# Kernel optimization log

Hardware: AMD Instinct MI355X
Metric: run time of the kernel (lower is better)

## Reference

```python
import jax, jax.numpy as jnp
import numpy as np

PRE_NMS_TOPK = 6000
POST_NMS_TOPK = 1000
NMS_THRESH = 0.7
MIN_SIZE = 16.0
N = 1_000_000
H, W = 800, 1333


def setup_inputs() -> dict:
    key = jax.random.key(0)
    ki, kx, ky, kw, kh, kd, kl = jax.random.split(key, 7)
    image = jax.random.normal(ki, (1, H, W, 3), jnp.float32)
    # realistic anchors: centers uniform over image, sizes in [8, 228)
    cx = jax.random.uniform(kx, (N,), jnp.float32) * W
    cy = jax.random.uniform(ky, (N,), jnp.float32) * H
    aw = jax.random.uniform(kw, (N,), jnp.float32) * 220.0 + 8.0
    ah = jax.random.uniform(kh, (N,), jnp.float32) * 220.0 + 8.0
    anchors = jnp.stack([cx - 0.5 * aw, cy - 0.5 * ah, cx + 0.5 * aw, cy + 0.5 * ah], axis=1)
    bbox_deltas = jax.random.normal(kd, (N, 4), jnp.float32) * 0.1
    logits = jax.random.normal(kl, (N, 1), jnp.float32)
    return {"image": image, "anchors": anchors, "bbox_deltas": bbox_deltas, "logits": logits}


def _iou_matrix(boxes):
    # boxes: [K,4] as (x1,y1,x2,y2); IoU is symmetric in axis labeling,
    # matching tf.image.non_max_suppression's overlap math.
    x1, y1, x2, y2 = boxes[:, 0], boxes[:, 1], boxes[:, 2], boxes[:, 3]
    area = (x2 - x1) * (y2 - y1)
    ix1 = jnp.maximum(x1[:, None], x1[None, :])
    iy1 = jnp.maximum(y1[:, None], y1[None, :])
    ix2 = jnp.minimum(x2[:, None], x2[None, :])
    iy2 = jnp.minimum(y2[:, None], y2[None, :])
    inter = jnp.maximum(ix2 - ix1, 0.0) * jnp.maximum(iy2 - iy1, 0.0)
    union = area[:, None] + area[None, :] - inter
    return jnp.where(union > 0.0, inter / union, 0.0)


def _sequential_nms(iou, valid, thresh):
    # iou: [K,K]; boxes are already sorted by descending score.
    K = iou.shape[0]
    idx = jnp.arange(K)

    def step(keep, inp):
        i, row = inp
        ki = keep[i]
        suppress = ki & (row > thresh) & (idx > i)
        return keep & ~suppress, ki

    _, kept = jax.lax.scan(step, valid, (idx, iou))
    return kept  # [K] bool, in sorted order


def reference(image, anchors, bbox_deltas, logits):
    height = jnp.float32(image.shape[1])
    width = jnp.float32(image.shape[2])

    # --- box decode ---
    wa = anchors[:, 2] - anchors[:, 0]
    ha = anchors[:, 3] - anchors[:, 1]
    xa = anchors[:, 0] + 0.5 * wa
    ya = anchors[:, 1] + 0.5 * ha
    x = bbox_deltas[:, 0] * wa + xa
    y = bbox_deltas[:, 1] * ha + ya
    w = jnp.exp(bbox_deltas[:, 2]) * wa
    h = jnp.exp(bbox_deltas[:, 3]) * ha
    x1 = jnp.clip(x - 0.5 * w, 0.0, width - 1.0)
    y1 = jnp.clip(y - 0.5 * h, 0.0, height - 1.0)
    x2 = jnp.clip(x + 0.5 * w, 0.0, width - 1.0)
    y2 = jnp.clip(y + 0.5 * h, 0.0, height - 1.0)
    proposals = jnp.stack([x1, y1, x2, y2], axis=1)  # [N,4]

    # --- min-size filter (mask instead of dynamic gather) ---
    valid = ((x2 - x1) >= MIN_SIZE) & ((y2 - y1) >= MIN_SIZE)
    scores = jnp.where(valid, jax.nn.sigmoid(logits[:, 0]), -jnp.inf)

    # --- pre-NMS top-k ---
    top_scores, top_idx = jax.lax.top_k(scores, PRE_NMS_TOPK)
    top_boxes = proposals[top_idx]              # [K,4]
    top_valid = top_scores > -jnp.inf

    # --- NMS ---
    iou = _iou_matrix(top_boxes)
    kept = _sequential_nms(iou, top_valid, NMS_THRESH)

    # --- pack kept boxes (in score order) into fixed [POST,4], zero-padded ---
    rank = jnp.cumsum(kept.astype(jnp.int32)) - 1
    slot = jnp.where(kept, rank, POST_NMS_TOPK)  # invalid -> dropped
    out = jnp.zeros((POST_NMS_TOPK, 4), top_boxes.dtype)
    out = out.at[slot].set(top_boxes, mode="drop")
    return out
```

## Files before the change

kernel.cpp:

```cpp
#include <hip/hip_runtime.h>
#include <stdint.h>
#include <math.h>

#define N_ANCH   1000000
#define N4       (N_ANCH / 4)
#define NBLK4    ((N4 + 1023) / 1024)
#define NBLK256  ((N4 + 255) / 256)
#define PRE_K    6000
#define POST_K   1000
#define WORDS    94
#define ROWS     6016
#define W_IMG    1333.0f
#define H_IMG    800.0f

#define NS       7168
#define RBLK     112

#define OFF_KEYS   0x000000u
#define OFF_HIST1  0x400000u
#define OFF_HIST2  0x404000u
#define OFF_CTRL   0x410000u
#define OFF_CAND   0x410100u
#define OFF_BOXES  0x41F000u
#define OFF_VALID  0x437000u
#define OFF_MASK   0x440000u

__device__ __forceinline__ float ref_exp(float v) {
  return (float)exp((double)v);
}

__device__ __forceinline__ void decode_box(float ax, float ay, float az, float aw,
                                           float dx, float dy, float dz, float dw,
                                           float& x1, float& y1, float& x2, float& y2,
                                           bool& valid) {
  float wa = __fsub_rn(az, ax);
  float ha = __fsub_rn(aw, ay);
  float xa = __fadd_rn(ax, __fmul_rn(0.5f, wa));
  float ya = __fadd_rn(ay, __fmul_rn(0.5f, ha));
  float x  = __fadd_rn(__fmul_rn(dx, wa), xa);
  float y  = __fadd_rn(__fmul_rn(dy, ha), ya);
  float w  = __fmul_rn(ref_exp(dz), wa);
  float h  = __fmul_rn(ref_exp(dw), ha);
  float hw = __fmul_rn(0.5f, w);
  float hh = __fmul_rn(0.5f, h);
  x1 = fminf(fmaxf(__fsub_rn(x, hw), 0.0f), W_IMG - 1.0f);
  y1 = fminf(fmaxf(__fsub_rn(y, hh), 0.0f), H_IMG - 1.0f);
  x2 = fminf(fmaxf(__fadd_rn(x, hw), 0.0f), W_IMG - 1.0f);
  y2 = fminf(fmaxf(__fadd_rn(y, hh), 0.0f), H_IMG - 1.0f);
  valid = (__fsub_rn(x2, x1) >= 16.0f) && (__fsub_rn(y2, y1) >= 16.0f);
}

__device__ __forceinline__ uint32_t wave_iscan(uint32_t x, int lane) {
  #pragma unroll
  for (int off = 1; off < 64; off <<= 1) {
    uint32_t u = __shfl_up(x, off, 64);
    if (lane >= off) x += u;
  }
  return x;
}

__device__ __forceinline__ uint64_t bcast64(uint64_t v, int lane) {
  uint32_t lo = (uint32_t)__builtin_amdgcn_readlane((int)(uint32_t)v, lane);
  uint32_t hi = (uint32_t)__builtin_amdgcn_readlane((int)(uint32_t)(v >> 32), lane);
  return ((uint64_t)hi << 32) | lo;
}

__global__ void __launch_bounds__(256) k_decode(const float4* __restrict__ anchors,
                                                const float4* __restrict__ deltas,
                                                const float*  __restrict__ logits,
                                                uint32_t* __restrict__ keys) {
  int i = blockIdx.x * 256 + threadIdx.x;
  if (i >= N_ANCH) return;
  float4 a = anchors[i];
  float4 d = deltas[i];
  float wa = a.z - a.x, ha = a.w - a.y;
  float xa = a.x + 0.5f * wa, ya = a.y + 0.5f * ha;
  float x = d.x * wa + xa, y = d.y * ha + ya;
  float w = __expf(d.z) * wa, h = __expf(d.w) * ha;
  float fx1 = fminf(fmaxf(x - 0.5f * w, 0.0f), W_IMG - 1.0f);
  float fx2 = fminf(fmaxf(x + 0.5f * w, 0.0f), W_IMG - 1.0f);
  float fy1 = fminf(fmaxf(y - 0.5f * h, 0.0f), H_IMG - 1.0f);
  float fy2 = fminf(fmaxf(y + 0.5f * h, 0.0f), H_IMG - 1.0f);
  float X = fx2 - fx1, Y = fy2 - fy1;
  bool valid = (X >= 16.0f) && (Y >= 16.0f);
  if (fabsf(X - 16.0f) < 0.02f || fabsf(Y - 16.0f) < 0.02f) {
    float ex1, ey1, ex2, ey2; bool vv;
    decode_box(a.x, a.y, a.z, a.w, d.x, d.y, d.z, d.w, ex1, ey1, ex2, ey2, vv);
    valid = vv;
  }
  uint32_t u = __float_as_uint(logits[i]);
  uint32_t o = (u & 0x80000000u) ? ~u : (u | 0x80000000u);
  keys[i] = valid ? ~o : 0xFFFFFFFFu;
}

__global__ void __launch_bounds__(1024) k_histA(const uint4* __restrict__ keys4,
                                                uint32_t* __restrict__ hist1) {
  __shared__ uint32_t lh[4096];
  int tid = threadIdx.x, lane = tid & 63;
  for (int b = tid; b < 4096; b += 1024) lh[b] = 0u;
  __syncthreads();
  int i4 = blockIdx.x * 1024 + tid;
  uint32_t invc = 0;
  if (i4 < N4) {
    uint4 kk = keys4[i4];
    uint32_t ks[4] = { kk.x, kk.y, kk.z, kk.w };
    #pragma unroll
    for (int e = 0; e < 4; e++) {
      if (ks[e] != 0xFFFFFFFFu) atomicAdd(&lh[ks[e] >> 20], 1u);
      else invc++;
    }
  }
  #pragma unroll
  for (int off = 32; off > 0; off >>= 1) invc += __shfl_down(invc, off, 64);
  if (lane == 0 && invc) atomicAdd(&lh[4095], invc);
  __syncthreads();
  for (int b = tid; b < 4096; b += 1024) {
    uint32_t cv = lh[b];
    if (cv) atomicAdd(&hist1[b], cv);
  }
}

__global__ void __launch_bounds__(1024) k_cut1(const uint32_t* __restrict__ hist1,
                                               uint32_t* __restrict__ ctrl) {
  __shared__ uint32_t part[1024];
  int t = threadIdx.x;
  uint4 s4 = ((const uint4*)hist1)[t];
  uint32_t tot = s4.x + s4.y + s4.z + s4.w;
  part[t] = tot;
  __syncthreads();
  uint32_t inc = tot;
  for (int off = 1; off < 1024; off <<= 1) {
    uint32_t u = (t >= off) ? part[t - off] : 0u;
    __syncthreads();
    inc += u;
    part[t] = inc;
    __syncthreads();
  }
  uint32_t ex = inc - tot;
  if (ex < PRE_K && inc >= PRE_K) {
    uint32_t run = ex;
    uint32_t binv[4] = { s4.x, s4.y, s4.z, s4.w };
    for (int b = 0; b < 4; b++) {
      if (run + binv[b] >= PRE_K) { ctrl[2] = 4 * t + b; ctrl[3] = run; break; }
      run += binv[b];
    }
  }
  if (t == 1023 && inc < PRE_K) { ctrl[2] = 4095u; ctrl[3] = inc; }
}

__global__ void __launch_bounds__(256) k_hist2(const uint4* __restrict__ keys4,
                                               const uint32_t* __restrict__ ctrl,
                                               uint32_t* __restrict__ hist2) {
  __shared__ uint32_t lh[256];
  int tid = threadIdx.x;
  lh[tid] = 0u;
  __syncthreads();
  uint32_t c = ctrl[2];
  int i4 = blockIdx.x * 256 + tid;
  if (i4 < N4) {
    uint4 kk = keys4[i4];
    uint32_t ks[4] = { kk.x, kk.y, kk.z, kk.w };
    #pragma unroll
    for (int e = 0; e < 4; e++)
      if ((ks[e] >> 20) == c) atomicAdd(&lh[(ks[e] >> 12) & 0xFFu], 1u);
  }
  __syncthreads();
  uint32_t v = lh[tid];
  if (v) atomicAdd(&hist2[tid], v);
}

__global__ void __launch_bounds__(64) k_cut2(const uint32_t* __restrict__ hist2,
                                             uint32_t* __restrict__ ctrl) {
  int lane = threadIdx.x;
  uint32_t c = ctrl[2], base = ctrl[3];
  const uint32_t* p = hist2 + 4 * lane;
  uint32_t b0 = p[0], b1 = p[1], b2 = p[2], b3 = p[3];
  uint32_t tot = b0 + b1 + b2 + b3;
  uint32_t inc = wave_iscan(tot, lane);
  uint32_t ex = inc - tot;
  bool found = false;
  if (base + ex < PRE_K && base + inc >= PRE_K) {
    uint32_t run = base + ex;
    uint32_t binv[4] = { b0, b1, b2, b3 };
    for (int b = 0; b < 4; b++) {
      if (run + binv[b] >= PRE_K) { ctrl[1] = (c << 8) | (uint32_t)(4 * lane + b); found = true; break; }
      run += binv[b];
    }
  }
  uint64_t fb = __ballot(found);
  if (lane == 0 && fb == 0ull) ctrl[1] = 0xFFFFFu;
}

__global__ void __launch_bounds__(256) k_compact(const uint4* __restrict__ keys4,
                                                 const float* __restrict__ logits,
                                                 uint32_t* ctrl,
                                                 uint64_t* __restrict__ cand) {
  __shared__ uint32_t wcnt[4];
  __shared__ uint32_t bbase_s;
  int tid = threadIdx.x, lane = tid & 63, wv = tid >> 6;
  uint32_t T = ctrl[1];
  int i4 = blockIdx.x * 256 + tid;
  uint4 kk = make_uint4(~0u, ~0u, ~0u, ~0u);
  if (i4 < N4) kk = keys4[i4];
  uint32_t ks[4] = { kk.x, kk.y, kk.z, kk.w };
  bool pass[4]; uint64_t m[4];
  uint32_t tot = 0;
  #pragma unroll
  for (int e = 0; e < 4; e++) {
    pass[e] = (i4 < N4) && ((ks[e] >> 12) <= T);
    m[e] = __ballot(pass[e]);
    tot += (uint32_t)__popcll((unsigned long long)m[e]);
  }
  if (lane == 0) wcnt[wv] = tot;
  __syncthreads();
  if (tid == 0) {
    uint32_t bt = wcnt[0] + wcnt[1] + wcnt[2] + wcnt[3];
    bbase_s = bt ? atomicAdd(&ctrl[0], bt) : 0u;
  }
  __syncthreads();
  uint32_t wb = bbase_s;
  for (int w2 = 0; w2 < wv; w2++) wb += wcnt[w2];
  uint64_t lmask = (1ull << lane) - 1ull;
  #pragma unroll
  for (int e = 0; e < 4; e++) {
    if (pass[e]) {
      int i = 4 * i4 + e;
      uint32_t skey;
      if (ks[e] == 0xFFFFFFFFu) {
        skey = 0xFF800000u;
      } else {
        double xd = (double)logits[i];
        float s = (float)(1.0 / (1.0 + exp(-xd)));
        skey = 0x7FFFFFFFu & ~__float_as_uint(s);
      }
      uint32_t p = wb + (uint32_t)__popcll((unsigned long long)(m[e] & lmask));
      if (p < NS) cand[p] = ((uint64_t)skey << 20) | (uint32_t)i;
    }
    wb += (uint32_t)__popcll((unsigned long long)m[e]);
  }
}

__global__ void __launch_bounds__(256) k_rank(
    const uint32_t* __restrict__ ctrl,
    const uint64_t* __restrict__ cand,
    const float4* __restrict__ anchors,
    const float4* __restrict__ deltas,
    float4* __restrict__ boxes,
    uint32_t* __restrict__ valid) {
  __shared__ uint32_t part[4][64];
  int tid = threadIdx.x;
  int wv = tid >> 6, lane = tid & 63;
  int i = blockIdx.x * 64 + lane;
  uint32_t M = ctrl[0]; if (M > NS) M = NS;
  uint64_t myk = (i < (int)M) ? cand[i] : ~0ull;
  uint32_t cnt = 0;
  const int QUART = NS / 4;
  int jbase = wv * QUART;
  for (int s = 0; s < QUART / 64; s++) {
    int j = jbase + s * 64 + lane;
    uint64_t c = (j < (int)M) ? cand[j] : ~0ull;
    #pragma unroll
    for (int s2 = 0; s2 < 64; s2++) {
      uint64_t kb = bcast64(c, s2);
      cnt += (kb < myk) ? 1u : 0u;
    }
  }
  part[wv][lane] = cnt;
  __syncthreads();
  if (wv != 0) return;
  uint32_t rank = part[0][lane] + part[1][lane] + part[2][lane] + part[3][lane];
  if (i < (int)M && rank < PRE_K) {
    uint32_t skey = (uint32_t)(myk >> 20);
    uint32_t idx  = (uint32_t)(myk & 0xFFFFFu);
    if (skey >= 0xFF800000u) {
      boxes[rank] = make_float4(0.f, 0.f, 0.f, 0.f);
      valid[rank] = 0u;
    } else {
      float4 a = anchors[idx];
      float4 d = deltas[idx];
      float x1, y1, x2, y2; bool vv;
      decode_box(a.x, a.y, a.z, a.w, d.x, d.y, d.z, d.w, x1, y1, x2, y2, vv);
      boxes[rank] = make_float4(x1, y1, x2, y2);
      valid[rank] = 1u;
    }
  }
  if ((i >= (int)M || i >= PRE_K) && i < ROWS) {
    boxes[i] = make_float4(0.f, 0.f, 0.f, 0.f);
    valid[i] = 0u;
  }
}

__global__ void __launch_bounds__(64) k_iou(const float4* __restrict__ boxes,
                                            uint64_t* __restrict__ mask) {
  int by = blockIdx.y, bx = blockIdx.x;
  if (bx < by) return;
  __shared__ float4 cb[64];
  int t = threadIdx.x;
  cb[t] = boxes[bx * 64 + t];
  __syncthreads();
  int i = by * 64 + t;
  float4 b = boxes[i];
  float ax1 = b.x, ay1 = b.y, ax2 = b.z, ay2 = b.w;
  float areaA = __fmul_rn(__fsub_rn(ax2, ax1), __fsub_rn(ay2, ay1));
  uint64_t bits = 0;
  for (int c = 0; c < 64; c++) {
    float4 o = cb[c];
    float areaB = __fmul_rn(__fsub_rn(o.z, o.x), __fsub_rn(o.w, o.y));
    float ix1 = fmaxf(ax1, o.x), iy1 = fmaxf(ay1, o.y);
    float ix2 = fminf(ax2, o.z), iy2 = fminf(ay2, o.w);
    float iw = fmaxf(__fsub_rn(ix2, ix1), 0.0f);
    float ih = fmaxf(__fsub_rn(iy2, iy1), 0.0f);
    float inter = __fmul_rn(iw, ih);
    float uni = __fsub_rn(__fadd_rn(areaA, areaB), inter);
    bool sup = (uni > 0.0f) && (__fdiv_rn(inter, uni) > 0.7f);
    bits |= ((uint64_t)sup) << c;
  }
  mask[(size_t)i * WORDS + bx] = bits;
}

__global__ void __launch_bounds__(64, 1) k_nms(const uint64_t* __restrict__ mask,
                                               const float4* __restrict__ boxes,
                                               const uint32_t* __restrict__ valid,
                                               float* __restrict__ out) {
  __shared__ uint32_t list[1088];
  int lane = threadIdx.x;
  int wp = (2 * lane < WORDS) ? 2 * lane : 0;
  uint64_t rA = 0, rB = 0;
  int cnt = 0;
  uint64_t colv = mask[(size_t)lane * WORDS + 0];
  uint32_t vf = valid[lane];
  for (int g = 0; g < WORDS; g++) {
    int base = g * 64;
    uint64_t vA[64], vB[64];
    #pragma unroll
    for (int r = 0; r < 64; r++) {
      ulonglong2 t2 = *(const ulonglong2*)(mask + (size_t)(base + r) * WORDS + wp);
      vA[r] = t2.x; vB[r] = t2.y;
    }
    uint64_t colv_c = colv;
    uint32_t vf_c = vf;
    if (g + 1 < WORDS) {
      colv = mask[(size_t)(base + 64 + lane) * WORDS + (g + 1)];
      vf = valid[base + 64 + lane];
    }
    uint64_t cur = (g & 1) ? bcast64(rB, g >> 1) : bcast64(rA, g >> 1);
    uint64_t vmask = __ballot(vf_c != 0u);
    uint64_t alive = vmask & ~cur;
    uint64_t kept = 0;
    #pragma unroll
    for (int r = 0; r < 64; r++) {
      uint64_t mr = bcast64(colv_c, r);
      uint64_t take = (alive >> r) & 1ull;
      kept |= take << r;
      alive &= ~(take ? mr : 0ull);
    }
    uint32_t below = (uint32_t)__popcll((unsigned long long)(kept & ((1ull << lane) - 1ull)));
    if ((kept >> lane) & 1ull) {
      uint32_t pos = (uint32_t)cnt + below;
      if (pos < 1088u) list[pos] = (uint32_t)(base + lane);
    }
    cnt += (int)__popcll((unsigned long long)kept);
    if (cnt >= POST_K) break;
    if (g + 1 >= WORDS) break;
    uint64_t accA = 0, accB = 0;
    #pragma unroll
    for (int r = 0; r < 64; r++) {
      uint64_t s = 0ull - ((kept >> r) & 1ull);
      accA |= vA[r] & s;
      accB |= vB[r] & s;
    }
    rA |= accA;
    rB |= accB;
  }
  __syncthreads();
  float4* outv = (float4*)out;
  for (int k = lane; k < POST_K; k += 64)
    outv[k] = (k < cnt) ? boxes[list[k]] : make_float4(0.f, 0.f, 0.f, 0.f);
}

extern "C" void kernel_launch(void* const* d_in, const int* in_sizes, int n_in,
                              void* d_out, int out_size, void* d_ws, size_t ws_size,
                              hipStream_t stream) {
  const float4* anchors = (const float4*)d_in[1];
  const float4* deltas  = (const float4*)d_in[2];
  const float*  logits  = (const float*)d_in[3];
  char* w = (char*)d_ws;
  uint32_t* keys  = (uint32_t*)(w + OFF_KEYS);
  uint32_t* hist1 = (uint32_t*)(w + OFF_HIST1);
  uint32_t* hist2 = (uint32_t*)(w + OFF_HIST2);
  uint32_t* ctrl  = (uint32_t*)(w + OFF_CTRL);
  uint64_t* cand  = (uint64_t*)(w + OFF_CAND);
  float4*   boxes = (float4*)(w + OFF_BOXES);
  uint32_t* valid = (uint32_t*)(w + OFF_VALID);
  uint64_t* mask  = (uint64_t*)(w + OFF_MASK);
  float*    out   = (float*)d_out;

  hipMemsetAsync(w + OFF_HIST1, 0, 0x4400, stream);
  hipMemsetAsync(w + OFF_CTRL, 0, 256, stream);

  k_decode<<<(N_ANCH + 255) / 256, 256, 0, stream>>>(anchors, deltas, logits, keys);
  k_histA<<<NBLK4, 1024, 0, stream>>>((const uint4*)keys, hist1);
  k_cut1<<<1, 1024, 0, stream>>>(hist1, ctrl);
  k_hist2<<<NBLK256, 256, 0, stream>>>((const uint4*)keys, ctrl, hist2);
  k_cut2<<<1, 64, 0, stream>>>(hist2, ctrl);
  k_compact<<<NBLK256, 256, 0, stream>>>((const uint4*)keys, logits, ctrl, cand);
  k_rank<<<RBLK, 256, 0, stream>>>(ctrl, cand, anchors, deltas, boxes, valid);
  k_iou<<<dim3(WORDS, WORDS), 64, 0, stream>>>(boxes, mask);
  k_nms<<<1, 64, 0, stream>>>(mask, boxes, valid, out);
}
```

Before: 239.5 us.

## Split NMS suppression-row accumulation across four waves with shared-memory reduction

Measured after the change: 227.5 us. 5.0% less time.

```diff
diff --git a/kernel.cpp b/kernel.cpp
--- a/kernel.cpp
+++ b/kernel.cpp
@@ -15,6 +15,9 @@
 
 #define NS       7168
 #define RBLK     112
+
+#define NMS_WAVES 4
+#define RPW       16
 
 #define OFF_KEYS   0x000000u
 #define OFF_HIST1  0x400000u
@@ -318,24 +321,28 @@
   mask[(size_t)i * WORDS + bx] = bits;
 }
 
-__global__ void __launch_bounds__(64, 1) k_nms(const uint64_t* __restrict__ mask,
-                                               const float4* __restrict__ boxes,
-                                               const uint32_t* __restrict__ valid,
-                                               float* __restrict__ out) {
+__global__ void __launch_bounds__(256, 1) k_nms(const uint64_t* __restrict__ mask,
+                                                const float4* __restrict__ boxes,
+                                                const uint32_t* __restrict__ valid,
+                                                float* __restrict__ out) {
   __shared__ uint32_t list[1088];
-  int lane = threadIdx.x;
+  __shared__ uint64_t remS[2][NMS_WAVES];
+  int tid = threadIdx.x;
+  int lane = tid & 63, wv = tid >> 6;
   int wp = (2 * lane < WORDS) ? 2 * lane : 0;
   uint64_t rA = 0, rB = 0;
   int cnt = 0;
+  if (tid < 2 * NMS_WAVES) ((uint64_t*)remS)[tid] = 0ull;
   uint64_t colv = mask[(size_t)lane * WORDS + 0];
   uint32_t vf = valid[lane];
+  __syncthreads();
   for (int g = 0; g < WORDS; g++) {
     int base = g * 64;
-    uint64_t vA[64], vB[64];
-    #pragma unroll
-    for (int r = 0; r < 64; r++) {
-      ulonglong2 t2 = *(const ulonglong2*)(mask + (size_t)(base + r) * WORDS + wp);
-      vA[r] = t2.x; vB[r] = t2.y;
+    uint64_t vA[RPW], vB[RPW];
+    #pragma unroll
+    for (int k = 0; k < RPW; k++) {
+      ulonglong2 t2 = *(const ulonglong2*)(mask + (size_t)(base + wv * RPW + k) * WORDS + wp);
+      vA[k] = t2.x; vB[k] = t2.y;
     }
     uint64_t colv_c = colv;
     uint32_t vf_c = vf;
@@ -343,7 +350,7 @@
       colv = mask[(size_t)(base + 64 + lane) * WORDS + (g + 1)];
       vf = valid[base + 64 + lane];
     }
-    uint64_t cur = (g & 1) ? bcast64(rB, g >> 1) : bcast64(rA, g >> 1);
+    uint64_t cur = remS[g & 1][0] | remS[g & 1][1] | remS[g & 1][2] | remS[g & 1][3];
     uint64_t vmask = __ballot(vf_c != 0u);
     uint64_t alive = vmask & ~cur;
     uint64_t kept = 0;
@@ -354,27 +361,32 @@
       kept |= take << r;
       alive &= ~(take ? mr : 0ull);
     }
-    uint32_t below = (uint32_t)__popcll((unsigned long long)(kept & ((1ull << lane) - 1ull)));
-    if ((kept >> lane) & 1ull) {
-      uint32_t pos = (uint32_t)cnt + below;
-      if (pos < 1088u) list[pos] = (uint32_t)(base + lane);
+    if (wv == 0) {
+      uint32_t below = (uint32_t)__popcll((unsigned long long)(kept & ((1ull << lane) - 1ull)));
+      if ((kept >> lane) & 1ull) {
+        uint32_t pos = (uint32_t)cnt + below;
+        if (pos < 1088u) list[pos] = (uint32_t)(base + lane);
+      }
     }
     cnt += (int)__popcll((unsigned long long)kept);
     if (cnt >= POST_K) break;
     if (g + 1 >= WORDS) break;
     uint64_t accA = 0, accB = 0;
     #pragma unroll
-    for (int r = 0; r < 64; r++) {
-      uint64_t s = 0ull - ((kept >> r) & 1ull);
-      accA |= vA[r] & s;
-      accB |= vB[r] & s;
+    for (int k = 0; k < RPW; k++) {
+      uint64_t s = 0ull - ((kept >> (wv * RPW + k)) & 1ull);
+      accA |= vA[k] & s;
+      accB |= vB[k] & s;
     }
     rA |= accA;
     rB |= accB;
+    int nw = g + 1;
+    if (lane == (nw >> 1)) remS[nw & 1][wv] = (nw & 1) ? rB : rA;
+    __syncthreads();
   }
   __syncthreads();
   float4* outv = (float4*)out;
-  for (int k = lane; k < POST_K; k += 64)
+  for (int k = tid; k < POST_K; k += 256)
     outv[k] = (k < cnt) ? boxes[list[k]] : make_float4(0.f, 0.f, 0.f, 0.f);
 }
 
@@ -406,5 +418,5 @@
   k_compact<<<NBLK256, 256, 0, stream>>>((const uint4*)keys, logits, ctrl, cand);
   k_rank<<<RBLK, 256, 0, stream>>>(ctrl, cand, anchors, deltas, boxes, valid);
   k_iou<<<dim3(WORDS, WORDS), 64, 0, stream>>>(boxes, mask);
-  k_nms<<<1, 64, 0, stream>>>(mask, boxes, valid, out);
-}
+  k_nms<<<1, 256, 0, stream>>>(mask, boxes, valid, out);
+}
```

## Compute next NMS word suppression from kept-list gather instead of full row sweeps

Applied to the files above, without the earlier changes.

Result: no change. 238.4 us (-0.4%).

```diff
diff --git a/kernel.cpp b/kernel.cpp
--- a/kernel.cpp
+++ b/kernel.cpp
@@ -15,6 +15,8 @@
 
 #define NS       7168
 #define RBLK     112
+
+#define OLDK     16
 
 #define OFF_KEYS   0x000000u
 #define OFF_HIST1  0x400000u
@@ -62,6 +64,12 @@
 __device__ __forceinline__ uint64_t bcast64(uint64_t v, int lane) {
   uint32_t lo = (uint32_t)__builtin_amdgcn_readlane((int)(uint32_t)v, lane);
   uint32_t hi = (uint32_t)__builtin_amdgcn_readlane((int)(uint32_t)(v >> 32), lane);
+  return ((uint64_t)hi << 32) | lo;
+}
+
+__device__ __forceinline__ uint64_t shflxor64(uint64_t v, int m) {
+  uint32_t lo = (uint32_t)__shfl_xor((int)(uint32_t)v, m, 64);
+  uint32_t hi = (uint32_t)__shfl_xor((int)(uint32_t)(v >> 32), m, 64);
   return ((uint64_t)hi << 32) | lo;
 }
 
@@ -324,53 +332,59 @@
                                                float* __restrict__ out) {
   __shared__ uint32_t list[1088];
   int lane = threadIdx.x;
-  int wp = (2 * lane < WORDS) ? 2 * lane : 0;
-  uint64_t rA = 0, rB = 0;
+  uint64_t lmask = (1ull << lane) - 1ull;
   int cnt = 0;
   uint64_t colv = mask[(size_t)lane * WORDS + 0];
   uint32_t vf = valid[lane];
+  uint64_t cur = 0;
   for (int g = 0; g < WORDS; g++) {
     int base = g * 64;
-    uint64_t vA[64], vB[64];
-    #pragma unroll
-    for (int r = 0; r < 64; r++) {
-      ulonglong2 t2 = *(const ulonglong2*)(mask + (size_t)(base + r) * WORDS + wp);
-      vA[r] = t2.x; vB[r] = t2.y;
-    }
-    uint64_t colv_c = colv;
-    uint32_t vf_c = vf;
-    if (g + 1 < WORDS) {
-      colv = mask[(size_t)(base + 64 + lane) * WORDS + (g + 1)];
-      vf = valid[base + 64 + lane];
-    }
-    uint64_t cur = (g & 1) ? bcast64(rB, g >> 1) : bcast64(rA, g >> 1);
-    uint64_t vmask = __ballot(vf_c != 0u);
+    bool haveNext = (g + 1 < WORDS);
+    uint64_t newv = 0, colv_n = 0, oldv[OLDK];
+    uint32_t vf_n = 0, om = 0;
+    if (haveNext) {
+      newv   = mask[(size_t)(base + lane) * WORDS + (g + 1)];
+      colv_n = mask[(size_t)(base + 64 + lane) * WORDS + (g + 1)];
+      vf_n   = valid[base + 64 + lane];
+      #pragma unroll
+      for (int k = 0; k < OLDK; k++) {
+        int t = 64 * k + lane;
+        uint32_t row = (t < cnt) ? list[t] : 0u;
+        om |= (t < cnt) ? (1u << k) : 0u;
+        oldv[k] = mask[(size_t)row * WORDS + (g + 1)];
+      }
+    }
+    uint64_t vmask = __ballot(vf != 0u);
     uint64_t alive = vmask & ~cur;
     uint64_t kept = 0;
     #pragma unroll
     for (int r = 0; r < 64; r++) {
-      uint64_t mr = bcast64(colv_c, r);
+      uint64_t mr = bcast64(colv, r);
       uint64_t take = (alive >> r) & 1ull;
       kept |= take << r;
       alive &= ~(take ? mr : 0ull);
     }
-    uint32_t below = (uint32_t)__popcll((unsigned long long)(kept & ((1ull << lane) - 1ull)));
+    uint32_t below = (uint32_t)__popcll((unsigned long long)(kept & lmask));
     if ((kept >> lane) & 1ull) {
       uint32_t pos = (uint32_t)cnt + below;
       if (pos < 1088u) list[pos] = (uint32_t)(base + lane);
     }
     cnt += (int)__popcll((unsigned long long)kept);
-    if (cnt >= POST_K) break;
-    if (g + 1 >= WORDS) break;
-    uint64_t accA = 0, accB = 0;
-    #pragma unroll
-    for (int r = 0; r < 64; r++) {
-      uint64_t s = 0ull - ((kept >> r) & 1ull);
-      accA |= vA[r] & s;
-      accB |= vB[r] & s;
-    }
-    rA |= accA;
-    rB |= accB;
+    if (cnt >= POST_K || !haveNext) break;
+    asm volatile("" : "+v"(newv),
+                      "+v"(oldv[0]),  "+v"(oldv[1]),  "+v"(oldv[2]),  "+v"(oldv[3]),
+                      "+v"(oldv[4]),  "+v"(oldv[5]),  "+v"(oldv[6]),  "+v"(oldv[7]),
+                      "+v"(oldv[8]),  "+v"(oldv[9]),  "+v"(oldv[10]), "+v"(oldv[11]),
+                      "+v"(oldv[12]), "+v"(oldv[13]), "+v"(oldv[14]), "+v"(oldv[15]));
+    uint64_t acc = ((kept >> lane) & 1ull) ? newv : 0ull;
+    #pragma unroll
+    for (int k = 0; k < OLDK; k++)
+      acc |= oldv[k] & (0ull - (uint64_t)((om >> k) & 1u));
+    #pragma unroll
+    for (int off = 1; off < 64; off <<= 1)
+      acc |= shflxor64(acc, off);
+    cur = bcast64(acc, 0);
+    colv = colv_n; vf = vf_n;
   }
   __syncthreads();
   float4* outv = (float4*)out;
```
